# Performance work log

Hardware: AMD Instinct MI355X
Metric: run time of the kernel (lower is better)

The kernel has to match this reference:

```python
import jax, jax.numpy as jnp
import numpy as np

B, S, D_MODEL, H = 2, 2048, 1024, 16
HD = D_MODEL // H  # 64
THETA = 10000.0


def setup_inputs() -> dict:
    key = jax.random.key(0)
    ks = jax.random.split(key, 5)
    std = (2.0 / (D_MODEL + D_MODEL)) ** 0.5
    x = jax.random.normal(ks[0], (B, S, D_MODEL), dtype=jnp.float32)
    Wq = jax.random.normal(ks[1], (D_MODEL, D_MODEL), dtype=jnp.float32) * std
    Wk = jax.random.normal(ks[2], (D_MODEL, D_MODEL), dtype=jnp.float32) * std
    Wv = jax.random.normal(ks[3], (D_MODEL, D_MODEL), dtype=jnp.float32) * std
    Wo = jax.random.normal(ks[4], (D_MODEL, D_MODEL), dtype=jnp.float32) * std
    # RoPE tables (buffers)
    pos = jnp.arange(S, dtype=jnp.float32)
    freq = THETA ** (-jnp.arange(0, HD, 2, dtype=jnp.float32) / HD)  # [HD/2]
    ang = jnp.outer(pos, freq)  # [S, HD/2]
    token_positions = jnp.arange(S, dtype=jnp.int32)
    return {
        "x": x,
        "token_positions": token_positions,
        "use_rope": 1,
        "Wq": Wq, "Wk": Wk, "Wv": Wv, "Wo": Wo,
        "cos": jnp.cos(ang), "sin": jnp.sin(ang),
    }


def _apply_rope(t, c, sn):
    # t: [b,h,s,d]; c,sn: [s,d/2] (broadcast over b,h)
    e = t[..., 0::2]
    o = t[..., 1::2]
    return jnp.stack([e * c - o * sn, o * c + e * sn], axis=-1).reshape(t.shape)


def reference(x, token_positions, use_rope, Wq, Wk, Wv, Wo, cos, sin):
    b, s, _ = x.shape

    def split_heads(t):  # [b,s,D] -> [b,h,s,hd]
        return t.reshape(b, s, H, HD).transpose(0, 2, 1, 3)

    q = split_heads(x @ Wq.T)
    k = split_heads(x @ Wk.T)
    v = split_heads(x @ Wv.T)

    if use_rope:
        c = cos[token_positions]   # [s, hd/2]
        sn = sin[token_positions]  # [s, hd/2]
        q = _apply_rope(q, c, sn)
        k = _apply_rope(k, c, sn)

    scale = 1.0 / jnp.sqrt(jnp.float32(HD))
    scores = jnp.einsum('bhqd,bhkd->bhqk', q, k) * scale  # [b,h,s,s]
    causal = jnp.tril(jnp.ones((s, s), dtype=bool))
    scores = jnp.where(causal, scores, -jnp.inf)
    attn = jax.nn.softmax(scores, axis=-1)
    y = jnp.einsum('bhqk,bhkd->bhqd', attn, v)
    y = y.transpose(0, 2, 1, 3).reshape(b, s, D_MODEL)
    return y @ Wo.T
```

## Files before the change

kernel.cpp:

```cpp
#include <hip/hip_runtime.h>
#include <math.h>

#define BB 2
#define SS 2048
#define DM 1024
#define NH 16
#define HD 64

typedef __attribute__((ext_vector_type(8))) __bf16 bf16x8;
typedef __attribute__((ext_vector_type(4))) __bf16 bf16x4;
typedef __attribute__((ext_vector_type(8))) unsigned short u16x8;
typedef __attribute__((ext_vector_type(4))) float f32x4;
typedef unsigned short u16;
typedef unsigned int u32;
typedef __attribute__((address_space(1))) unsigned int u32g;
typedef __attribute__((address_space(3))) unsigned int u32l;

#define CEXP 0.18033688011112042f

static __device__ __forceinline__ u16 f2bf(float f) {
    __bf16 h = (__bf16)f;
    return __builtin_bit_cast(unsigned short, h);
}
static __device__ __forceinline__ float bfu2f(u16 v) {
    return __uint_as_float(((u32)v) << 16);
}

static __device__ __forceinline__ void gld16(const u16* g, u16* l) {
    __builtin_amdgcn_global_load_lds((const u32g*)g, (u32l*)l, 16, 0, 0);
}

__global__ __launch_bounds__(256)
void cast_all(const float* __restrict__ x,
              const float* __restrict__ wq, const float* __restrict__ wk,
              const float* __restrict__ wv, const float* __restrict__ wo,
              u16* __restrict__ xb, u16* __restrict__ wqb, u16* __restrict__ wkb,
              u16* __restrict__ wvb, u16* __restrict__ wob)
{
    const int N4X = (BB * SS * DM) / 4;
    const int N4W = (DM * DM) / 4;
    int i = blockIdx.x * 256 + threadIdx.x;
    const float* src; u16* dst; int off;
    if (i < N4X) { src = x; dst = xb; off = i; }
    else {
        int i2 = i - N4X;
        int w = i2 >> 18;
        off = i2 & (N4W - 1);
        switch (w) {
            case 0:  src = wq; dst = wqb; break;
            case 1:  src = wk; dst = wkb; break;
            case 2:  src = wv; dst = wvb; break;
            default: src = wo; dst = wob; break;
        }
    }
    float4 v = ((const float4*)src)[off];
    ushort4 o;
    o.x = f2bf(v.x); o.y = f2bf(v.y); o.z = f2bf(v.z); o.w = f2bf(v.w);
    ((ushort4*)dst)[off] = o;
}

__global__ __launch_bounds__(256, 3)
void qkv_gemm(const u16* __restrict__ X,
              const u16* __restrict__ Wq, const u16* __restrict__ Wk,
              const u16* __restrict__ Wv,
              const int* __restrict__ tp, const float* __restrict__ cosp,
              const float* __restrict__ sinp, const int* __restrict__ use_rope,
              u16* __restrict__ Q, u16* __restrict__ K, u16* __restrict__ V)
{
    const u16* W; u16* dst;
    if (blockIdx.z == 0)      { W = Wq; dst = Q; }
    else if (blockIdx.z == 1) { W = Wk; dst = K; }
    else                      { W = Wv; dst = V; }

    __shared__ u16 SH[4 * 64 * 68];
    u16* As = SH;
    u16* Bs = SH + 8192;
    const int t  = threadIdx.x;
    const int wv = t >> 6, L = t & 63, ln = L & 15, qd = L >> 4;
    const int i0 = blockIdx.y * 128, j0 = blockIdx.x * 128;
    const int wm = (wv >> 1) * 64, wn = (wv & 1) * 64;
    const int srow = L >> 3;
    const int scg  = ((L & 7) ^ (L >> 3)) * 8;

    f32x4 acc[4][4];
    #pragma unroll
    for (int a = 0; a < 4; ++a)
        #pragma unroll
        for (int b = 0; b < 4; ++b)
            #pragma unroll
            for (int e = 0; e < 4; ++e) acc[a][b][e] = 0.f;

    for (int k0 = 0; k0 < DM; k0 += 64) {
        __syncthreads();
        #pragma unroll
        for (int g = 0; g < 4; ++g) {
            int rb = wv * 32 + g * 8;
            gld16(X + (size_t)(i0 + rb + srow) * DM + k0 + scg, &As[rb * 64]);
            gld16(W + (size_t)(j0 + rb + srow) * DM + k0 + scg, &Bs[rb * 64]);
        }
        __syncthreads();
        bf16x8 a[4][2], b[4][2];
        #pragma unroll
        for (int mi = 0; mi < 4; ++mi)
            #pragma unroll
            for (int kd = 0; kd < 2; ++kd)
                a[mi][kd] = *(const bf16x8*)&As[(wm + mi * 16 + ln) * 64 + (((kd * 4 + qd) ^ (ln & 7)) * 8)];
        #pragma unroll
        for (int ni = 0; ni < 4; ++ni)
            #pragma unroll
            for (int kd = 0; kd < 2; ++kd)
                b[ni][kd] = *(const bf16x8*)&Bs[(wn + ni * 16 + ln) * 64 + (((kd * 4 + qd) ^ (ln & 7)) * 8)];
        #pragma unroll
        for (int kd = 0; kd < 2; ++kd)
            #pragma unroll
            for (int mi = 0; mi < 4; ++mi)
                #pragma unroll
                for (int ni = 0; ni < 4; ++ni)
                    acc[mi][ni] = __builtin_amdgcn_mfma_f32_16x16x32_bf16(a[mi][kd], b[ni][kd], acc[mi][ni], 0, 0, 0);
    }

    __syncthreads();
    u16* Ts = SH + wv * (64 * 68);
    #pragma unroll
    for (int mi = 0; mi < 4; ++mi)
        #pragma unroll
        for (int ni = 0; ni < 4; ++ni)
            #pragma unroll
            for (int r = 0; r < 4; ++r)
                Ts[(mi * 16 + qd * 4 + r) * 68 + ni * 16 + ln] = f2bf(acc[mi][ni][r]);

    const int rope_on = (blockIdx.z < 2) ? use_rope[0] : 0;
    const int h  = blockIdx.x * 2 + (wv & 1);
    const int sb = i0 + wm;
    const int lrow = L >> 3, lcol = (L & 7) * 8;
    #pragma unroll
    for (int r2 = 0; r2 < 8; ++r2) {
        int row = lrow + r2 * 8;
        u16x8 val = *(const u16x8*)&Ts[row * 68 + lcol];
        int sg = sb + row;
        int b_ = sg >> 11, s = sg & 2047;
        if (rope_on) {
            int pos = tp[s];
            float cc[4], sc[4];
            *(float4*)cc = *(const float4*)&cosp[pos * 32 + (lcol >> 1)];
            *(float4*)sc = *(const float4*)&sinp[pos * 32 + (lcol >> 1)];
            #pragma unroll
            for (int j = 0; j < 4; ++j) {
                float e = bfu2f(val[2 * j]), o = bfu2f(val[2 * j + 1]);
                val[2 * j]     = f2bf(e * cc[j] - o * sc[j]);
                val[2 * j + 1] = f2bf(o * cc[j] + e * sc[j]);
            }
        }
        *(u16x8*)&dst[(((size_t)(b_ * NH + h)) * SS + s) * HD + lcol] = val;
    }
}

__global__ __launch_bounds__(256, 2)
void out_gemm(const u16* __restrict__ X, const u16* __restrict__ W,
              float* __restrict__ dst)
{
    __shared__ char SHB[36864];
    u16* As = (u16*)SHB;
    u16* Bs = (u16*)SHB + 8192;
    const int t  = threadIdx.x;
    const int wv = t >> 6, L = t & 63, ln = L & 15, qd = L >> 4;
    const int i0 = blockIdx.y * 128, j0 = blockIdx.x * 64;
    const int wm = (wv >> 1) * 64, wn = (wv & 1) * 32;
    const int srow = L >> 3;
    const int scg  = ((L & 7) ^ (L >> 3)) * 8;

    f32x4 acc[4][2];
    #pragma unroll
    for (int mi = 0; mi < 4; ++mi)
        #pragma unroll
        for (int ni = 0; ni < 2; ++ni)
            #pragma unroll
            for (int e = 0; e < 4; ++e) acc[mi][ni][e] = 0.f;

    for (int k0 = 0; k0 < DM; k0 += 64) {
        __syncthreads();
        #pragma unroll
        for (int g = 0; g < 4; ++g) {
            int rb = wv * 32 + g * 8;
            gld16(X + (size_t)(i0 + rb + srow) * DM + k0 + scg, &As[rb * 64]);
        }
        #pragma unroll
        for (int g = 0; g < 2; ++g) {
            int rb = wv * 16 + g * 8;
            gld16(W + (size_t)(j0 + rb + srow) * DM + k0 + scg, &Bs[rb * 64]);
        }
        __syncthreads();
        bf16x8 a[4][2], b[2][2];
        #pragma unroll
        for (int mi = 0; mi < 4; ++mi)
            #pragma unroll
            for (int kd = 0; kd < 2; ++kd)
                a[mi][kd] = *(const bf16x8*)&As[(wm + mi * 16 + ln) * 64 + (((kd * 4 + qd) ^ (ln & 7)) * 8)];
        #pragma unroll
        for (int ni = 0; ni < 2; ++ni)
            #pragma unroll
            for (int kd = 0; kd < 2; ++kd)
                b[ni][kd] = *(const bf16x8*)&Bs[(wn + ni * 16 + ln) * 64 + (((kd * 4 + qd) ^ (ln & 7)) * 8)];
        #pragma unroll
        for (int kd = 0; kd < 2; ++kd)
            #pragma unroll
            for (int mi = 0; mi < 4; ++mi)
                #pragma unroll
                for (int ni = 0; ni < 2; ++ni)
                    acc[mi][ni] = __builtin_amdgcn_mfma_f32_16x16x32_bf16(a[mi][kd], b[ni][kd], acc[mi][ni], 0, 0, 0);
    }

    __syncthreads();
    float* Ts = (float*)SHB + wv * (64 * 36);
    #pragma unroll
    for (int mi = 0; mi < 4; ++mi)
        #pragma unroll
        for (int ni = 0; ni < 2; ++ni)
            #pragma unroll
            for (int r = 0; r < 4; ++r)
                Ts[(mi * 16 + qd * 4 + r) * 36 + ni * 16 + ln] = acc[mi][ni][r];

    const int lrow = L >> 3, lch = L & 7;
    #pragma unroll
    for (int r2 = 0; r2 < 8; ++r2) {
        int row = lrow + r2 * 8;
        float4 v = *(const float4*)&Ts[row * 36 + lch * 4];
        *(float4*)&dst[(size_t)(i0 + wm + row) * DM + j0 + wn + lch * 4] = v;
    }
}

static __device__ __forceinline__ void step128(
    const u16* KsB, const bf16x8 qf[2], u16* psw,
    bool mask, int rowg, int j0, int ln, int qd,
    float& m, float& l, f32x4* o, bf16x8 pf[4])
{
    f32x4 s[8];
    #pragma unroll
    for (int mt = 0; mt < 8; ++mt) {
        bf16x8 a0 = *(const bf16x8*)&KsB[(mt * 16 + ln) * 64 + ((qd ^ (ln & 7)) * 8)];
        bf16x8 a1 = *(const bf16x8*)&KsB[(mt * 16 + ln) * 64 + (((4 + qd) ^ (ln & 7)) * 8)];
        #pragma unroll
        for (int e = 0; e < 4; ++e) s[mt][e] = 0.f;
        s[mt] = __builtin_amdgcn_mfma_f32_16x16x32_bf16(a0, qf[0], s[mt], 0, 0, 0);
        s[mt] = __builtin_amdgcn_mfma_f32_16x16x32_bf16(a1, qf[1], s[mt], 0, 0, 0);
    }
    if (mask) {
        #pragma unroll
        for (int mt = 0; mt < 8; ++mt)
            #pragma unroll
            for (int r = 0; r < 4; ++r)
                if (j0 + mt * 16 + qd * 4 + r > rowg) s[mt][r] = -3.0e38f;
    }
    float rm = s[0][0];
    #pragma unroll
    for (int mt = 0; mt < 8; ++mt)
        #pragma unroll
        for (int r = 0; r < 4; ++r) rm = fmaxf(rm, s[mt][r]);
    rm = fmaxf(rm, __shfl_xor(rm, 16));
    rm = fmaxf(rm, __shfl_xor(rm, 32));
    float nm = fmaxf(m, rm);
    float alpha = exp2f((m - nm) * CEXP);
    float nmc = nm * CEXP;
    float rs = 0.f;
    #pragma unroll
    for (int mt = 0; mt < 8; ++mt) {
        bf16x4 pk;
        #pragma unroll
        for (int r = 0; r < 4; ++r) {
            float pv = exp2f(fmaf(s[mt][r], CEXP, -nmc));
            rs += pv;
            pk[r] = (__bf16)pv;
        }
        *(bf16x4*)(psw + ln * 136 + mt * 16 + qd * 4) = pk;
    }
    rs += __shfl_xor(rs, 16);
    rs += __shfl_xor(rs, 32);
    l = l * alpha + rs;
    m = nm;
    #pragma unroll
    for (int r = 0; r < 4; ++r) {
        float ar = __shfl(alpha, qd * 4 + r);
        #pragma unroll
        for (int ni = 0; ni < 4; ++ni) o[ni][r] *= ar;
    }
    #pragma unroll
    for (int kc = 0; kc < 4; ++kc)
        pf[kc] = *(const bf16x8*)(psw + ln * 136 + kc * 32 + qd * 8);
}

__global__ __launch_bounds__(256, 2)
void attn_kernel(const u16* __restrict__ Q, const u16* __restrict__ K,
                 const u16* __restrict__ V, u16* __restrict__ Y)
{
    __shared__ u16 Ks[128 * 64];
    __shared__ u16 Vt[64 * 128];
    __shared__ u16 Ps[4][16 * 136];

    const int t  = threadIdx.x;
    const int wv = t >> 6, L = t & 63, ln = L & 15, qd = L >> 4;
    const int bh = blockIdx.x, p = blockIdx.y;
    const int qbA = p * 64, qbB = (31 - p) * 64;
    const int cA = (p >> 1) + 1;
    const int ntile = (33 - p) >> 1;
    const u16* Qp = Q + (size_t)bh * SS * HD;
    const u16* Kp = K + (size_t)bh * SS * HD;
    const u16* Vp = V + (size_t)bh * SS * HD;
    const int srow = L >> 3;
    const int scg  = ((L & 7) ^ (L >> 3)) * 8;
    const int vkp = t & 63;
    const int vdg0 = t >> 6;

    bf16x8 qfA[2], qfB[2];
    {
        const u16* ra = Qp + (size_t)(qbA + wv * 16 + ln) * HD;
        qfA[0] = *(const bf16x8*)(ra + qd * 8);
        qfA[1] = *(const bf16x8*)(ra + 32 + qd * 8);
        const u16* rb = Qp + (size_t)(qbB + wv * 16 + ln) * HD;
        qfB[0] = *(const bf16x8*)(rb + qd * 8);
        qfB[1] = *(const bf16x8*)(rb + 32 + qd * 8);
    }

    f32x4 oA[4], oB[4];
    #pragma unroll
    for (int ni = 0; ni < 4; ++ni)
        #pragma unroll
        for (int e = 0; e < 4; ++e) { oA[ni][e] = 0.f; oB[ni][e] = 0.f; }
    float mA = -3.0e38f, lA = 0.f, mB = -3.0e38f, lB = 0.f;

    for (int tix = 0; tix < ntile; ++tix) {
        const int j0 = tix * 128;
        __syncthreads();
        #pragma unroll
        for (int g = 0; g < 4; ++g) {
            int rb = wv * 32 + g * 8;
            gld16(Kp + (size_t)(j0 + rb + srow) * HD + scg, &Ks[rb * 64]);
        }
        #pragma unroll
        for (int vvp = 0; vvp < 2; ++vvp) {
            int dg = vdg0 + 4 * vvp;
            const u16* v0 = Vp + (size_t)(j0 + 2 * vkp) * HD + dg * 8;
            u16x8 va = *(const u16x8*)v0;
            u16x8 vb = *(const u16x8*)(v0 + HD);
            #pragma unroll
            for (int u = 0; u < 8; ++u) {
                int d = dg * 8 + u;
                u32 w = (u32)va[u] | ((u32)vb[u] << 16);
                *(u32*)&Vt[d * 128 + (((vkp >> 2) ^ (d & 7)) * 8) + 2 * (vkp & 3)] = w;
            }
        }
        __syncthreads();

        const bool hasA = (tix < cA);
        bf16x8 pA[4], pB[4];
        if (hasA)
            step128(Ks, qfA, &Ps[wv][0], tix == cA - 1, qbA + wv * 16 + ln, j0, ln, qd,
                    mA, lA, oA, pA);
        step128(Ks, qfB, &Ps[wv][0], tix == ntile - 1, qbB + wv * 16 + ln, j0, ln, qd,
                mB, lB, oB, pB);

        #pragma unroll
        for (int kc = 0; kc < 4; ++kc)
            #pragma unroll
            for (int ni = 0; ni < 4; ++ni) {
                bf16x8 vf = *(const bf16x8*)&Vt[(ni * 16 + ln) * 128 + (((kc * 4 + qd) ^ (ln & 7)) * 8)];
                if (hasA)
                    oA[ni] = __builtin_amdgcn_mfma_f32_16x16x32_bf16(pA[kc], vf, oA[ni], 0, 0, 0);
                oB[ni] = __builtin_amdgcn_mfma_f32_16x16x32_bf16(pB[kc], vf, oB[ni], 0, 0, 0);
            }
    }

    const int b = bh >> 4, h = bh & 15;
    #pragma unroll
    for (int r = 0; r < 4; ++r) {
        float invA = 1.f / __shfl(lA, qd * 4 + r);
        float invB = 1.f / __shfl(lB, qd * 4 + r);
        int sA = qbA + wv * 16 + qd * 4 + r;
        int sB = qbB + wv * 16 + qd * 4 + r;
        #pragma unroll
        for (int ni = 0; ni < 4; ++ni) {
            int d = ni * 16 + ln;
            Y[((size_t)(b * SS + sA)) * DM + h * HD + d] = f2bf(oA[ni][r] * invA);
            Y[((size_t)(b * SS + sB)) * DM + h * HD + d] = f2bf(oB[ni][r] * invB);
        }
    }
}

extern "C" void kernel_launch(void* const* d_in, const int* in_sizes, int n_in,
                              void* d_out, int out_size, void* d_ws, size_t ws_size,
                              hipStream_t stream)
{
    const float* x        = (const float*)d_in[0];
    const int*   tp       = (const int*)d_in[1];
    const int*   use_rope = (const int*)d_in[2];
    const float* Wq       = (const float*)d_in[3];
    const float* Wk       = (const float*)d_in[4];
    const float* Wv       = (const float*)d_in[5];
    const float* Wo       = (const float*)d_in[6];
    const float* cosp     = (const float*)d_in[7];
    const float* sinp     = (const float*)d_in[8];
    float* out = (float*)d_out;

    char* ws = (char*)d_ws;
    const size_t MB = 1 << 20;
    u16* xb  = (u16*)(ws);
    u16* Wqb = (u16*)(ws + 8 * MB);
    u16* Wkb = (u16*)(ws + 10 * MB);
    u16* Wvb = (u16*)(ws + 12 * MB);
    u16* Wob = (u16*)(ws + 14 * MB);
    u16* Qb  = (u16*)(ws + 16 * MB);
    u16* Kb  = (u16*)(ws + 24 * MB);
    u16* Vb  = (u16*)(ws + 32 * MB);
    u16* Yb  = (u16*)(ws + 40 * MB);

    cast_all<<<8192, 256, 0, stream>>>(x, Wq, Wk, Wv, Wo, xb, Wqb, Wkb, Wvb, Wob);
    qkv_gemm<<<dim3(DM / 128, BB * SS / 128, 3), 256, 0, stream>>>(
        xb, Wqb, Wkb, Wvb, tp, cosp, sinp, use_rope, Qb, Kb, Vb);
    attn_kernel<<<dim3(BB * NH, 16), 256, 0, stream>>>(Qb, Kb, Vb, Yb);
    out_gemm<<<dim3(DM / 64, BB * SS / 128), 256, 0, stream>>>(Yb, Wob, out);
}
```

Measured before the change: 196.4 us.

## Double-buffer 64-key K/V tiles in attention and apply RoPE in registers

The attention kernel now uses 64-key tiles with double-buffered K and V in shared memory. The next tile is prefetched (K via global_load_lds, V into registers then transposed into LDS) while the current tile is computed, and there is a single barrier per iteration. Smaller tiles also trim masked work on the diagonal and reduce LDS footprint. Separately, RoPE in the QKV GEMM epilogue is applied to fp32 accumulators with lane shuffles before bf16 rounding, which changes rounding slightly and adds per-element scalar cos/sin loads.

```diff
diff --git a/kernel.cpp b/kernel.cpp
--- a/kernel.cpp
+++ b/kernel.cpp
@@ -21,9 +21,6 @@
 static __device__ __forceinline__ u16 f2bf(float f) {
     __bf16 h = (__bf16)f;
     return __builtin_bit_cast(unsigned short, h);
-}
-static __device__ __forceinline__ float bfu2f(u16 v) {
-    return __uint_as_float(((u32)v) << 16);
 }
 
 static __device__ __forceinline__ void gld16(const u16* g, u16* l) {
@@ -119,6 +116,28 @@
                     acc[mi][ni] = __builtin_amdgcn_mfma_f32_16x16x32_bf16(a[mi][kd], b[ni][kd], acc[mi][ni], 0, 0, 0);
     }
 
+    const int rope_on = (blockIdx.z < 2) ? use_rope[0] : 0;
+    if (rope_on) {
+        #pragma unroll
+        for (int mi = 0; mi < 4; ++mi)
+            #pragma unroll
+            for (int r = 0; r < 4; ++r) {
+                int gi = i0 + wm + mi * 16 + qd * 4 + r;
+                int s = gi & 2047;
+                int pos = tp[s];
+                #pragma unroll
+                for (int ni = 0; ni < 4; ++ni) {
+                    int d = wn + ni * 16 + ln;
+                    int dh = d & 63;
+                    float c  = cosp[pos * 32 + (dh >> 1)];
+                    float sn = sinp[pos * 32 + (dh >> 1)];
+                    float v = acc[mi][ni][r];
+                    float pv = __shfl_xor(v, 1);
+                    acc[mi][ni][r] = (dh & 1) ? (v * c + pv * sn) : (v * c - pv * sn);
+                }
+            }
+    }
+
     __syncthreads();
     u16* Ts = SH + wv * (64 * 68);
     #pragma unroll
@@ -129,7 +148,6 @@
             for (int r = 0; r < 4; ++r)
                 Ts[(mi * 16 + qd * 4 + r) * 68 + ni * 16 + ln] = f2bf(acc[mi][ni][r]);
 
-    const int rope_on = (blockIdx.z < 2) ? use_rope[0] : 0;
     const int h  = blockIdx.x * 2 + (wv & 1);
     const int sb = i0 + wm;
     const int lrow = L >> 3, lcol = (L & 7) * 8;
@@ -139,18 +157,6 @@
         u16x8 val = *(const u16x8*)&Ts[row * 68 + lcol];
         int sg = sb + row;
         int b_ = sg >> 11, s = sg & 2047;
-        if (rope_on) {
-            int pos = tp[s];
-            float cc[4], sc[4];
-            *(float4*)cc = *(const float4*)&cosp[pos * 32 + (lcol >> 1)];
-            *(float4*)sc = *(const float4*)&sinp[pos * 32 + (lcol >> 1)];
-            #pragma unroll
-            for (int j = 0; j < 4; ++j) {
-                float e = bfu2f(val[2 * j]), o = bfu2f(val[2 * j + 1]);
-                val[2 * j]     = f2bf(e * cc[j] - o * sc[j]);
-                val[2 * j + 1] = f2bf(o * cc[j] + e * sc[j]);
-            }
-        }
         *(u16x8*)&dst[(((size_t)(b_ * NH + h)) * SS + s) * HD + lcol] = val;
     }
 }
@@ -229,14 +235,14 @@
     }
 }
 
-static __device__ __forceinline__ void step128(
+static __device__ __forceinline__ void group_step(
     const u16* KsB, const bf16x8 qf[2], u16* psw,
-    bool mask, int rowg, int j0, int ln, int qd,
-    float& m, float& l, f32x4* o, bf16x8 pf[4])
-{
-    f32x4 s[8];
-    #pragma unroll
-    for (int mt = 0; mt < 8; ++mt) {
+    bool diag, int rowg, int j0, int ln, int qd,
+    float& m, float& l, f32x4* o, bf16x8& pf0, bf16x8& pf1)
+{
+    f32x4 s[4];
+    #pragma unroll
+    for (int mt = 0; mt < 4; ++mt) {
         bf16x8 a0 = *(const bf16x8*)&KsB[(mt * 16 + ln) * 64 + ((qd ^ (ln & 7)) * 8)];
         bf16x8 a1 = *(const bf16x8*)&KsB[(mt * 16 + ln) * 64 + (((4 + qd) ^ (ln & 7)) * 8)];
         #pragma unroll
@@ -244,16 +250,16 @@
         s[mt] = __builtin_amdgcn_mfma_f32_16x16x32_bf16(a0, qf[0], s[mt], 0, 0, 0);
         s[mt] = __builtin_amdgcn_mfma_f32_16x16x32_bf16(a1, qf[1], s[mt], 0, 0, 0);
     }
-    if (mask) {
-        #pragma unroll
-        for (int mt = 0; mt < 8; ++mt)
+    if (diag) {
+        #pragma unroll
+        for (int mt = 0; mt < 4; ++mt)
             #pragma unroll
             for (int r = 0; r < 4; ++r)
                 if (j0 + mt * 16 + qd * 4 + r > rowg) s[mt][r] = -3.0e38f;
     }
     float rm = s[0][0];
     #pragma unroll
-    for (int mt = 0; mt < 8; ++mt)
+    for (int mt = 0; mt < 4; ++mt)
         #pragma unroll
         for (int r = 0; r < 4; ++r) rm = fmaxf(rm, s[mt][r]);
     rm = fmaxf(rm, __shfl_xor(rm, 16));
@@ -263,7 +269,7 @@
     float nmc = nm * CEXP;
     float rs = 0.f;
     #pragma unroll
-    for (int mt = 0; mt < 8; ++mt) {
+    for (int mt = 0; mt < 4; ++mt) {
         bf16x4 pk;
         #pragma unroll
         for (int r = 0; r < 4; ++r) {
@@ -271,7 +277,7 @@
             rs += pv;
             pk[r] = (__bf16)pv;
         }
-        *(bf16x4*)(psw + ln * 136 + mt * 16 + qd * 4) = pk;
+        *(bf16x4*)(psw + ln * 72 + mt * 16 + qd * 4) = pk;
     }
     rs += __shfl_xor(rs, 16);
     rs += __shfl_xor(rs, 32);
@@ -283,32 +289,28 @@
         #pragma unroll
         for (int ni = 0; ni < 4; ++ni) o[ni][r] *= ar;
     }
-    #pragma unroll
-    for (int kc = 0; kc < 4; ++kc)
-        pf[kc] = *(const bf16x8*)(psw + ln * 136 + kc * 32 + qd * 8);
+    pf0 = *(const bf16x8*)(psw + ln * 72 + qd * 8);
+    pf1 = *(const bf16x8*)(psw + ln * 72 + 32 + qd * 8);
 }
 
 __global__ __launch_bounds__(256, 2)
 void attn_kernel(const u16* __restrict__ Q, const u16* __restrict__ K,
                  const u16* __restrict__ V, u16* __restrict__ Y)
 {
-    __shared__ u16 Ks[128 * 64];
-    __shared__ u16 Vt[64 * 128];
-    __shared__ u16 Ps[4][16 * 136];
+    __shared__ u16 Ks[2][64 * 64];
+    __shared__ u16 Vt[2][64 * 64];
+    __shared__ u16 Ps[4][16 * 72];
 
     const int t  = threadIdx.x;
     const int wv = t >> 6, L = t & 63, ln = L & 15, qd = L >> 4;
     const int bh = blockIdx.x, p = blockIdx.y;
     const int qbA = p * 64, qbB = (31 - p) * 64;
-    const int cA = (p >> 1) + 1;
-    const int ntile = (33 - p) >> 1;
     const u16* Qp = Q + (size_t)bh * SS * HD;
     const u16* Kp = K + (size_t)bh * SS * HD;
     const u16* Vp = V + (size_t)bh * SS * HD;
     const int srow = L >> 3;
     const int scg  = ((L & 7) ^ (L >> 3)) * 8;
-    const int vkp = t & 63;
-    const int vdg0 = t >> 6;
+    const int vkp = t & 31, vdg = t >> 5;
 
     bf16x8 qfA[2], qfB[2];
     {
@@ -327,46 +329,65 @@
         for (int e = 0; e < 4; ++e) { oA[ni][e] = 0.f; oB[ni][e] = 0.f; }
     float mA = -3.0e38f, lA = 0.f, mB = -3.0e38f, lB = 0.f;
 
+    const int ntile = 32 - p;
+
+    gld16(Kp + (size_t)(wv * 16 +     srow) * HD + scg, &Ks[0][(wv * 16    ) * 64]);
+    gld16(Kp + (size_t)(wv * 16 + 8 + srow) * HD + scg, &Ks[0][(wv * 16 + 8) * 64]);
+    {
+        const u16* v0 = Vp + (size_t)(2 * vkp) * HD + vdg * 8;
+        u16x8 va = *(const u16x8*)v0;
+        u16x8 vb = *(const u16x8*)(v0 + HD);
+        #pragma unroll
+        for (int u = 0; u < 8; ++u) {
+            int d = vdg * 8 + u;
+            u32 w = (u32)va[u] | ((u32)vb[u] << 16);
+            *(u32*)&Vt[0][d * 64 + ((vkp >> 2) ^ (d & 7)) * 8 + 2 * (vkp & 3)] = w;
+        }
+    }
+    __syncthreads();
+
     for (int tix = 0; tix < ntile; ++tix) {
-        const int j0 = tix * 128;
+        const int j0 = tix * 64;
+        const int buf = tix & 1;
+        const bool more = (tix + 1 < ntile);
+
+        u16x8 nva, nvb;
+        if (more) {
+            const int j1 = j0 + 64;
+            gld16(Kp + (size_t)(j1 + wv * 16 +     srow) * HD + scg, &Ks[buf ^ 1][(wv * 16    ) * 64]);
+            gld16(Kp + (size_t)(j1 + wv * 16 + 8 + srow) * HD + scg, &Ks[buf ^ 1][(wv * 16 + 8) * 64]);
+            const u16* v1 = Vp + (size_t)(j1 + 2 * vkp) * HD + vdg * 8;
+            nva = *(const u16x8*)v1;
+            nvb = *(const u16x8*)(v1 + HD);
+        }
+
+        const bool hasA = (tix <= p);
+        bf16x8 pA0, pA1, pB0, pB1;
+        if (hasA)
+            group_step(Ks[buf], qfA, &Ps[wv][0], tix == p, qbA + wv * 16 + ln, j0, ln, qd,
+                       mA, lA, oA, pA0, pA1);
+        group_step(Ks[buf], qfB, &Ps[wv][0], tix == ntile - 1, qbB + wv * 16 + ln, j0, ln, qd,
+                   mB, lB, oB, pB0, pB1);
+
+        #pragma unroll
+        for (int kc = 0; kc < 2; ++kc)
+            #pragma unroll
+            for (int ni = 0; ni < 4; ++ni) {
+                bf16x8 vf = *(const bf16x8*)&Vt[buf][(ni * 16 + ln) * 64 + (((kc * 4 + qd) ^ (ln & 7)) * 8)];
+                if (hasA)
+                    oA[ni] = __builtin_amdgcn_mfma_f32_16x16x32_bf16(kc ? pA1 : pA0, vf, oA[ni], 0, 0, 0);
+                oB[ni] = __builtin_amdgcn_mfma_f32_16x16x32_bf16(kc ? pB1 : pB0, vf, oB[ni], 0, 0, 0);
+            }
+
+        if (more) {
+            #pragma unroll
+            for (int u = 0; u < 8; ++u) {
+                int d = vdg * 8 + u;
+                u32 w = (u32)nva[u] | ((u32)nvb[u] << 16);
+                *(u32*)&Vt[buf ^ 1][d * 64 + ((vkp >> 2) ^ (d & 7)) * 8 + 2 * (vkp & 3)] = w;
+            }
+        }
         __syncthreads();
-        #pragma unroll
-        for (int g = 0; g < 4; ++g) {
-            int rb = wv * 32 + g * 8;
-            gld16(Kp + (size_t)(j0 + rb + srow) * HD + scg, &Ks[rb * 64]);
-        }
-        #pragma unroll
-        for (int vvp = 0; vvp < 2; ++vvp) {
-            int dg = vdg0 + 4 * vvp;
-            const u16* v0 = Vp + (size_t)(j0 + 2 * vkp) * HD + dg * 8;
-            u16x8 va = *(const u16x8*)v0;
-            u16x8 vb = *(const u16x8*)(v0 + HD);
-            #pragma unroll
-            for (int u = 0; u < 8; ++u) {
-                int d = dg * 8 + u;
-                u32 w = (u32)va[u] | ((u32)vb[u] << 16);
-                *(u32*)&Vt[d * 128 + (((vkp >> 2) ^ (d & 7)) * 8) + 2 * (vkp & 3)] = w;
-            }
-        }
-        __syncthreads();
-
-        const bool hasA = (tix < cA);
-        bf16x8 pA[4], pB[4];
-        if (hasA)
-            step128(Ks, qfA, &Ps[wv][0], tix == cA - 1, qbA + wv * 16 + ln, j0, ln, qd,
-                    mA, lA, oA, pA);
-        step128(Ks, qfB, &Ps[wv][0], tix == ntile - 1, qbB + wv * 16 + ln, j0, ln, qd,
-                mB, lB, oB, pB);
-
-        #pragma unroll
-        for (int kc = 0; kc < 4; ++kc)
-            #pragma unroll
-            for (int ni = 0; ni < 4; ++ni) {
-                bf16x8 vf = *(const bf16x8*)&Vt[(ni * 16 + ln) * 128 + (((kc * 4 + qd) ^ (ln & 7)) * 8)];
-                if (hasA)
-                    oA[ni] = __builtin_amdgcn_mfma_f32_16x16x32_bf16(pA[kc], vf, oA[ni], 0, 0, 0);
-                oB[ni] = __builtin_amdgcn_mfma_f32_16x16x32_bf16(pB[kc], vf, oB[ni], 0, 0, 0);
-            }
     }
 
     const int b = bh >> 4, h = bh & 15;
```

Result: no change. 193.4 us (-1.5%).
